# Kernel optimization log

Hardware: AMD Instinct MI355X
Metric: run time of the kernel (lower is better)

## Reference

```python
import jax, jax.numpy as jnp
import numpy as np

N_CODES = 1024  # 'N' in the module: number of codebook entries
DIM = 128       # 'K' in the module: embedding dimension


def setup_inputs() -> dict:
    key = jax.random.key(0)
    k1, k2 = jax.random.split(key)
    x = jax.random.normal(k1, (32, 64, 64, DIM), dtype=jnp.float32)
    # tf.random_uniform_initializer default: uniform in [-0.05, 0.05)
    codebook = jax.random.uniform(k2, (DIM, N_CODES), dtype=jnp.float32,
                                  minval=-0.05, maxval=0.05)
    return {"x": x, "codebook": codebook}


def reference(x, codebook):
    # x: [B, H, W, K]; codebook: [K, N] (codes are columns)
    K = codebook.shape[0]
    flat = x.reshape(-1, K)  # [M, K]
    sim = flat @ codebook    # [M, N]
    dist = (jnp.sum(flat * flat, axis=1, keepdims=True)
            + jnp.sum(codebook * codebook, axis=0)
            - 2.0 * sim)
    idx = jnp.argmin(dist, axis=1)                      # [M]
    q = jnp.take(codebook.T, idx, axis=0).reshape(x.shape)  # gather columns
    # straight-through estimator
    return x + jax.lax.stop_gradient(q - x)
```

## Files before the change

kernel.cpp:

```cpp
#include <hip/hip_runtime.h>
#include <math.h>

typedef _Float16 half8 __attribute__((ext_vector_type(8)));
typedef float    f32x4 __attribute__((ext_vector_type(4)));

#define DIM     128
#define NCODES  1024
#define M_ROWS  (32*64*64)
#define MTILE   128
#define NCHUNK  64
#define M_TEST  3.0e-3f
#define WL_CAP  16384
#define GR      64
#define CSTR    132

__device__ __forceinline__ float sqf(float v) {
    return (float)((double)v * (double)v);
}

__global__ void vq_prep(const float* __restrict__ cb,
                        float* __restrict__ cbT,
                        _Float16* __restrict__ ch,
                        float* __restrict__ cc,
                        int* __restrict__ cnt,
                        unsigned long long* __restrict__ bst) {
    const int b = blockIdx.x;
    if (b < 512) {
        int e = b * 256 + threadIdx.x;
        int n = e & 1023, k = e >> 10;
        float v = cb[k * NCODES + n];
        cbT[n * DIM + k] = v;
        ch[n * DIM + k]  = (_Float16)v;
    } else if (b < 516) {
        int n = (b - 512) * 256 + threadIdx.x;
        float acc = 0.f;
        for (int k = 0; k < DIM; ++k)
            acc = acc + sqf(cb[k * NCODES + n]);
        cc[n] = acc;
        if (n == 0) *cnt = 0;
    } else {
        int s = (b - 516) * 256 + threadIdx.x;
        bst[s] = 0xFFFFFFFFFFFFFFFFull;
    }
}

__device__ __forceinline__ void stage_chunk(const _Float16* __restrict__ ch,
                                            _Float16* lds,
                                            int chunk, int w, int quad, int lane15) {
#pragma unroll
    for (int i = 0; i < 4; ++i) {
        int r = (w << 4) + (i << 2) + quad;
        const _Float16* g = ch + (size_t)(chunk * NCHUNK + r) * DIM
                               + ((lane15 ^ (r & 7)) << 3);
        __builtin_amdgcn_global_load_lds(
            (const __attribute__((address_space(1))) void*)g,
            (__attribute__((address_space(3))) void*)(lds + (w << 11) + (i << 9)),
            16, 0, 0);
    }
}

__global__ __launch_bounds__(256, 2) void vq_gemm(const float* __restrict__ x,
                                                  const _Float16* __restrict__ ch,
                                                  const float* __restrict__ cc,
                                                  int* __restrict__ idx,
                                                  int* __restrict__ cnt,
                                                  int* __restrict__ wl) {
    __shared__ _Float16 bs[2][NCHUNK * DIM];
    __shared__ float ccL[NCODES];

    const int t      = threadIdx.x;
    const int w      = t >> 6;
    const int L      = t & 63;
    const int lane15 = L & 15;
    const int quad   = L >> 4;
    const int rowbase = blockIdx.x * MTILE + w * 32;

    stage_chunk(ch, bs[0], 0, w, quad, lane15);

#pragma unroll
    for (int i = 0; i < 4; ++i)
        ccL[t + 256 * i] = cc[t + 256 * i] + 4.0f;

    half8 af[2][4];
#pragma unroll
    for (int m = 0; m < 2; ++m) {
#pragma unroll
        for (int ks = 0; ks < 4; ++ks) {
            const float* src = x + (size_t)(rowbase + m * 16 + lane15) * DIM
                                 + ks * 32 + quad * 8;
            float4 f0 = *(const float4*)src;
            float4 f1 = *(const float4*)(src + 4);
            half8 h;
            h[0] = (_Float16)f0.x; h[1] = (_Float16)f0.y;
            h[2] = (_Float16)f0.z; h[3] = (_Float16)f0.w;
            h[4] = (_Float16)f1.x; h[5] = (_Float16)f1.y;
            h[6] = (_Float16)f1.z; h[7] = (_Float16)f1.w;
            af[m][ks] = h;
        }
    }

    int roff[4];
#pragma unroll
    for (int ks = 0; ks < 4; ++ks)
        roff[ks] = lane15 * DIM + ((((ks << 2) + quad) ^ (lane15 & 7)) << 3);

    unsigned p1[2][4], p2[2][4];
#pragma unroll
    for (int m = 0; m < 2; ++m)
#pragma unroll
        for (int r = 0; r < 4; ++r) { p1[m][r] = 0xFFFFFFFFu; p2[m][r] = 0xFFFFFFFFu; }

    __syncthreads();

    for (int c = 0; c < NCODES / NCHUNK; ++c) {
        if (c + 1 < NCODES / NCHUNK)
            stage_chunk(ch, bs[(c + 1) & 1], c + 1, w, quad, lane15);

        float cc4[4];
#pragma unroll
        for (int j = 0; j < 4; ++j)
            cc4[j] = ccL[c * NCHUNK + j * 16 + lane15];

        const _Float16* bp = bs[c & 1];
        f32x4 acc[2][4];
#pragma unroll
        for (int m = 0; m < 2; ++m)
#pragma unroll
            for (int j = 0; j < 4; ++j) {
                f32x4 z = {0.f, 0.f, 0.f, 0.f};
                acc[m][j] = z;
            }

#pragma unroll
        for (int ks = 0; ks < 4; ++ks) {
            half8 bf[4];
#pragma unroll
            for (int j = 0; j < 4; ++j)
                bf[j] = *(const half8*)(bp + (j << 11) + roff[ks]);
#pragma unroll
            for (int j = 0; j < 4; ++j)
#pragma unroll
                for (int m = 0; m < 2; ++m)
                    acc[m][j] = __builtin_amdgcn_mfma_f32_16x16x32_f16(af[m][ks], bf[j], acc[m][j], 0, 0, 0);
        }

#pragma unroll
        for (int j = 0; j < 4; ++j) {
            int col = c * NCHUNK + j * 16 + lane15;
#pragma unroll
            for (int m = 0; m < 2; ++m)
#pragma unroll
                for (int r = 0; r < 4; ++r) {
                    float s = fmaf(-2.0f, acc[m][j][r], cc4[j]);
                    s = fmaxf(s, 0.25f);
                    unsigned up = (__float_as_uint(s) & 0xFFFFFC00u) | (unsigned)col;
                    unsigned a  = p1[m][r];
                    unsigned lo = a < up ? a : up;
                    unsigned hi = a < up ? up : a;
                    p1[m][r] = lo;
                    p2[m][r] = p2[m][r] < hi ? p2[m][r] : hi;
                }
        }
        __syncthreads();
    }

#pragma unroll
    for (int m = 0; m < 2; ++m)
#pragma unroll
        for (int r = 0; r < 4; ++r) {
            unsigned a1 = p1[m][r], a2 = p2[m][r];
#pragma unroll
            for (int mask = 1; mask <= 8; mask <<= 1) {
                unsigned b1 = (unsigned)__shfl_xor((int)a1, mask, 64);
                unsigned b2 = (unsigned)__shfl_xor((int)a2, mask, 64);
                unsigned n1 = a1 < b1 ? a1 : b1;
                unsigned hi = a1 < b1 ? b1 : a1;
                unsigned mn = a2 < b2 ? a2 : b2;
                unsigned n2 = hi < mn ? hi : mn;
                a1 = n1; a2 = n2;
            }
            if (lane15 == 0) {
                int row = rowbase + m * 16 + quad * 4 + r;
                idx[row] = (int)(a1 & 0x3FFu);
                float s1 = __uint_as_float(a1 & 0xFFFFFC00u);
                float s2 = __uint_as_float(a2 & 0xFFFFFC00u);
                if (s2 - s1 < M_TEST) {
                    int slot = atomicAdd(cnt, 1);
                    if (slot < WL_CAP) wl[slot] = row;
                }
            }
        }
}

__global__ __launch_bounds__(256, 2) void vq_exact(const float* __restrict__ x,
                                                   const float* __restrict__ cbT,
                                                   const float* __restrict__ cc,
                                                   const int* __restrict__ cnt,
                                                   const int* __restrict__ wl,
                                                   unsigned long long* __restrict__ bst) {
    __shared__ float xsS[GR * CSTR];
    __shared__ float cbS[64 * CSTR];
    __shared__ float xxS[GR];

    const int t  = threadIdx.x;
    const int r4 = t >> 4;
    const int q  = t & 15;

    int count = *cnt;
    if (count > WL_CAP) count = WL_CAP;
    const int ngrp   = (count + GR - 1) / GR;
    const int nitems = ngrp * 4;

    for (int it = blockIdx.x; it < nitems; it += gridDim.x) {
        const int grp = it >> 2;
        const int cq  = it & 3;

        __syncthreads();
#pragma unroll
        for (int j = 0; j < 8; ++j) {
            int e  = t + 256 * j;
            int rr = e >> 5, k4 = e & 31;
            int sl = grp * GR + rr;
            sl = sl < count ? sl : count - 1;
            int rw = wl[sl];
            float4 v = ((const float4*)x)[(size_t)rw * 32 + k4];
            *(float4*)&xsS[rr * CSTR + k4 * 4] = v;
        }
        __syncthreads();

        if (t < GR) {
            const float* xs = &xsS[t * CSTR];
            float r0 = sqf(xs[0]), r1 = sqf(xs[1]), r2 = sqf(xs[2]), r3 = sqf(xs[3]);
            float r4_ = sqf(xs[4]), r5 = sqf(xs[5]), r6 = sqf(xs[6]), r7 = sqf(xs[7]);
#pragma unroll
            for (int k = 8; k < DIM; k += 8) {
                r0 = r0 + sqf(xs[k + 0]); r1 = r1 + sqf(xs[k + 1]);
                r2 = r2 + sqf(xs[k + 2]); r3 = r3 + sqf(xs[k + 3]);
                r4_ = r4_ + sqf(xs[k + 4]); r5 = r5 + sqf(xs[k + 5]);
                r6 = r6 + sqf(xs[k + 6]); r7 = r7 + sqf(xs[k + 7]);
            }
            xxS[t] = ((r0 + r1) + (r2 + r3)) + ((r4_ + r5) + (r6 + r7));
        }
        __syncthreads();

        float xxv[4];
#pragma unroll
        for (int i = 0; i < 4; ++i) xxv[i] = xxS[r4 * 4 + i];

        unsigned long long best[4];
#pragma unroll
        for (int i = 0; i < 4; ++i) best[i] = 0xFFFFFFFFFFFFFFFFull;

        for (int ch = 0; ch < 4; ++ch) {
            const int nb = cq * 256 + ch * 64;
            __syncthreads();
#pragma unroll
            for (int j = 0; j < 8; ++j) {
                int e  = t + 256 * j;
                int ci = e >> 5, k4 = e & 31;
                float4 v = ((const float4*)cbT)[(size_t)(nb + ci) * 32 + k4];
                *(float4*)&cbS[ci * CSTR + k4 * 4] = v;
            }
            __syncthreads();

            float a[4][4];
#pragma unroll
            for (int i = 0; i < 4; ++i)
#pragma unroll
                for (int j = 0; j < 4; ++j) a[i][j] = 0.f;

#pragma unroll 4
            for (int k4 = 0; k4 < 32; ++k4) {
                float4 xv[4], cv[4];
#pragma unroll
                for (int i = 0; i < 4; ++i)
                    xv[i] = *(const float4*)&xsS[(r4 * 4 + i) * CSTR + k4 * 4];
#pragma unroll
                for (int j = 0; j < 4; ++j)
                    cv[j] = *(const float4*)&cbS[(q + 16 * j) * CSTR + k4 * 4];
#pragma unroll
                for (int i = 0; i < 4; ++i)
#pragma unroll
                    for (int j = 0; j < 4; ++j) {
                        float acc = a[i][j];
                        acc = fmaf(cv[j].x, xv[i].x, acc);
                        acc = fmaf(cv[j].y, xv[i].y, acc);
                        acc = fmaf(cv[j].z, xv[i].z, acc);
                        acc = fmaf(cv[j].w, xv[i].w, acc);
                        a[i][j] = acc;
                    }
            }

#pragma unroll
            for (int j = 0; j < 4; ++j) {
                int n = nb + q + 16 * j;
                float ccn = cc[n];
#pragma unroll
                for (int i = 0; i < 4; ++i) {
                    float tt = xxv[i] + ccn;
                    float d  = tt - (a[i][j] + a[i][j]);
                    unsigned u  = __float_as_uint(d);
                    unsigned mk = (unsigned)(((int)u) >> 31);
                    unsigned f  = u ^ (mk | 0x80000000u);
                    unsigned long long key = ((unsigned long long)f << 32) | (unsigned)n;
                    best[i] = key < best[i] ? key : best[i];
                }
            }
        }

#pragma unroll
        for (int i = 0; i < 4; ++i) {
            unsigned long long b = best[i];
#pragma unroll
            for (int mask = 1; mask <= 8; mask <<= 1) {
                unsigned long long o =
                    (unsigned long long)__shfl_xor((long long)b, mask, 64);
                b = o < b ? o : b;
            }
            if (q == 0) {
                int sl = grp * GR + r4 * 4 + i;
                if (sl < count) atomicMin(&bst[sl], b);
            }
        }
    }
}

__global__ void vq_fix(const int* __restrict__ cnt,
                       const int* __restrict__ wl,
                       const unsigned long long* __restrict__ bst,
                       int* __restrict__ idx) {
    int count = *cnt;
    if (count > WL_CAP) count = WL_CAP;
    for (int s = blockIdx.x * 256 + threadIdx.x; s < count; s += gridDim.x * 256)
        idx[wl[s]] = (int)(bst[s] & 0xFFFFFFFFull);
}

__global__ void vq_out(const float* __restrict__ cbT,
                       const int* __restrict__ idx,
                       float* __restrict__ out) {
    size_t e = (size_t)blockIdx.x * 256 + threadIdx.x;
    int row = (int)(e >> 5);
    int k4  = (int)(e & 31);
    ((float4*)out)[e] = ((const float4*)cbT)[(size_t)idx[row] * 32 + k4];
}

extern "C" void kernel_launch(void* const* d_in, const int* in_sizes, int n_in,
                              void* d_out, int out_size, void* d_ws, size_t ws_size,
                              hipStream_t stream) {
    const float* x  = (const float*)d_in[0];
    const float* cb = (const float*)d_in[1];
    float* out = (float*)d_out;

    char* p = (char*)d_ws;
    float*    cbT = (float*)p;               p += NCODES * DIM * sizeof(float);
    _Float16* ch  = (_Float16*)p;            p += NCODES * DIM * sizeof(_Float16);
    float*    cc  = (float*)p;               p += NCODES * sizeof(float);
    int*      idx = (int*)p;                 p += M_ROWS * sizeof(int);
    int*      cnt = (int*)p;                 p += 16 * sizeof(int);
    int*      wl  = (int*)p;                 p += WL_CAP * sizeof(int);
    unsigned long long* bst = (unsigned long long*)p;

    vq_prep<<<580, 256, 0, stream>>>(cb, cbT, ch, cc, cnt, bst);
    vq_gemm<<<M_ROWS / MTILE, 256, 0, stream>>>(x, ch, cc, idx, cnt, wl);
    vq_exact<<<512, 256, 0, stream>>>(x, cbT, cc, cnt, wl, bst);
    vq_fix<<<64, 256, 0, stream>>>(cnt, wl, bst, idx);
    vq_out<<<(M_ROWS * (DIM / 4)) / 256, 256, 0, stream>>>(cbT, idx, out);
}
```

Measured before the change: 186.1 us.

## Software-pipeline MFMA chains with epilogue of previous chunk in vq_gemm

Restructures the codebook chunk loop so the MFMA chain for chunk c+1 is issued before the argmin epilogue of chunk c, using two accumulator sets. This lets the scalar compare/min work overlap with matrix-core latency instead of serializing after it. The ccL table is permuted so each lane reads its four per-chunk norms with one float4 LDS load. The vq_exact grid is doubled. Two accumulator sets raise register pressure, which could limit occupancy at two blocks per CU.

Measured after the change: 196.1 us. +5.4%, slower.

```diff
diff --git a/kernel.cpp b/kernel.cpp
--- a/kernel.cpp
+++ b/kernel.cpp
@@ -59,6 +59,55 @@
     }
 }
 
+#define ZACC(A)                                                               \
+    _Pragma("unroll")                                                         \
+    for (int m_ = 0; m_ < 2; ++m_)                                            \
+        _Pragma("unroll")                                                     \
+        for (int j_ = 0; j_ < 4; ++j_) {                                      \
+            f32x4 z_ = {0.f, 0.f, 0.f, 0.f};                                  \
+            A[m_][j_] = z_;                                                   \
+        }
+
+#define CHAIN(BP, A)                                                          \
+    _Pragma("unroll")                                                         \
+    for (int ks_ = 0; ks_ < 4; ++ks_) {                                       \
+        half8 bf_[4];                                                         \
+        _Pragma("unroll")                                                     \
+        for (int j_ = 0; j_ < 4; ++j_)                                        \
+            bf_[j_] = *(const half8*)((BP) + (j_ << 11) + roff[ks_]);         \
+        _Pragma("unroll")                                                     \
+        for (int j_ = 0; j_ < 4; ++j_)                                        \
+            _Pragma("unroll")                                                 \
+            for (int m_ = 0; m_ < 2; ++m_)                                    \
+                A[m_][j_] = __builtin_amdgcn_mfma_f32_16x16x32_f16(           \
+                    af[m_][ks_], bf_[j_], A[m_][j_], 0, 0, 0);                \
+    }
+
+#define EPI(A, CB, CC4)                                                       \
+    _Pragma("unroll")                                                         \
+    for (int j_ = 0; j_ < 4; ++j_) {                                          \
+        int col_ = (CB) * NCHUNK + j_ * 16 + lane15;                          \
+        _Pragma("unroll")                                                     \
+        for (int m_ = 0; m_ < 2; ++m_)                                        \
+            _Pragma("unroll")                                                 \
+            for (int r_ = 0; r_ < 4; ++r_) {                                  \
+                float s_ = fmaf(-2.0f, A[m_][j_][r_], CC4[j_]);               \
+                s_ = fmaxf(s_, 0.25f);                                        \
+                unsigned up_ = (__float_as_uint(s_) & 0xFFFFFC00u) | (unsigned)col_; \
+                unsigned a_  = p1[m_][r_];                                    \
+                unsigned lo_ = a_ < up_ ? a_ : up_;                           \
+                unsigned hi_ = a_ < up_ ? up_ : a_;                           \
+                p1[m_][r_] = lo_;                                             \
+                p2[m_][r_] = p2[m_][r_] < hi_ ? p2[m_][r_] : hi_;             \
+            }                                                                 \
+    }
+
+#define LOADCC(DST, C)                                                        \
+    {                                                                         \
+        float4 ccv_ = *(const float4*)&ccL[(((C) << 4) + lane15) << 2];       \
+        DST[0] = ccv_.x; DST[1] = ccv_.y; DST[2] = ccv_.z; DST[3] = ccv_.w;   \
+    }
+
 __global__ __launch_bounds__(256, 2) void vq_gemm(const float* __restrict__ x,
                                                   const _Float16* __restrict__ ch,
                                                   const float* __restrict__ cc,
@@ -78,8 +127,12 @@
     stage_chunk(ch, bs[0], 0, w, quad, lane15);
 
 #pragma unroll
-    for (int i = 0; i < 4; ++i)
-        ccL[t + 256 * i] = cc[t + 256 * i] + 4.0f;
+    for (int i = 0; i < 4; ++i) {
+        int e = t + 256 * i;
+        int c = e >> 6, rem = e & 63;
+        int l = rem >> 2, j = rem & 3;
+        ccL[e] = cc[c * 64 + j * 16 + l] + 4.0f;
+    }
 
     half8 af[2][4];
 #pragma unroll
@@ -112,57 +165,36 @@
 
     __syncthreads();
 
-    for (int c = 0; c < NCODES / NCHUNK; ++c) {
-        if (c + 1 < NCODES / NCHUNK)
-            stage_chunk(ch, bs[(c + 1) & 1], c + 1, w, quad, lane15);
-
-        float cc4[4];
-#pragma unroll
-        for (int j = 0; j < 4; ++j)
-            cc4[j] = ccL[c * NCHUNK + j * 16 + lane15];
-
-        const _Float16* bp = bs[c & 1];
-        f32x4 acc[2][4];
-#pragma unroll
-        for (int m = 0; m < 2; ++m)
-#pragma unroll
-            for (int j = 0; j < 4; ++j) {
-                f32x4 z = {0.f, 0.f, 0.f, 0.f};
-                acc[m][j] = z;
-            }
-
-#pragma unroll
-        for (int ks = 0; ks < 4; ++ks) {
-            half8 bf[4];
-#pragma unroll
-            for (int j = 0; j < 4; ++j)
-                bf[j] = *(const half8*)(bp + (j << 11) + roff[ks]);
-#pragma unroll
-            for (int j = 0; j < 4; ++j)
-#pragma unroll
-                for (int m = 0; m < 2; ++m)
-                    acc[m][j] = __builtin_amdgcn_mfma_f32_16x16x32_f16(af[m][ks], bf[j], acc[m][j], 0, 0, 0);
-        }
-
-#pragma unroll
-        for (int j = 0; j < 4; ++j) {
-            int col = c * NCHUNK + j * 16 + lane15;
-#pragma unroll
-            for (int m = 0; m < 2; ++m)
-#pragma unroll
-                for (int r = 0; r < 4; ++r) {
-                    float s = fmaf(-2.0f, acc[m][j][r], cc4[j]);
-                    s = fmaxf(s, 0.25f);
-                    unsigned up = (__float_as_uint(s) & 0xFFFFFC00u) | (unsigned)col;
-                    unsigned a  = p1[m][r];
-                    unsigned lo = a < up ? a : up;
-                    unsigned hi = a < up ? up : a;
-                    p1[m][r] = lo;
-                    p2[m][r] = p2[m][r] < hi ? p2[m][r] : hi;
-                }
-        }
+    f32x4 accA[2][4], accB[2][4];
+    float cc4A[4], cc4B[4];
+
+    stage_chunk(ch, bs[1], 1, w, quad, lane15);
+    LOADCC(cc4A, 0);
+    ZACC(accA);
+    CHAIN(bs[0], accA);
+    __syncthreads();
+
+    for (int c = 1; c < 15; c += 2) {
+        stage_chunk(ch, bs[0], c + 1, w, quad, lane15);
+        LOADCC(cc4B, c);
+        ZACC(accB);
+        CHAIN(bs[1], accB);
+        EPI(accA, c - 1, cc4A);
         __syncthreads();
-    }
+
+        stage_chunk(ch, bs[1], c + 2, w, quad, lane15);
+        LOADCC(cc4A, c + 1);
+        ZACC(accA);
+        CHAIN(bs[0], accA);
+        EPI(accB, c, cc4B);
+        __syncthreads();
+    }
+
+    LOADCC(cc4B, 15);
+    ZACC(accB);
+    CHAIN(bs[1], accB);
+    EPI(accA, 14, cc4A);
+    EPI(accB, 15, cc4B);
 
 #pragma unroll
     for (int m = 0; m < 2; ++m)
@@ -362,7 +394,7 @@
 
     vq_prep<<<580, 256, 0, stream>>>(cb, cbT, ch, cc, cnt, bst);
     vq_gemm<<<M_ROWS / MTILE, 256, 0, stream>>>(x, ch, cc, idx, cnt, wl);
-    vq_exact<<<512, 256, 0, stream>>>(x, cbT, cc, cnt, wl, bst);
+    vq_exact<<<1024, 256, 0, stream>>>(x, cbT, cc, cnt, wl, bst);
     vq_fix<<<64, 256, 0, stream>>>(cnt, wl, bst, idx);
     vq_out<<<(M_ROWS * (DIM / 4)) / 256, 256, 0, stream>>>(cbT, idx, out);
 }
```

## Triple-buffer codebook chunks with one barrier per iteration and vectorized cc loads

Applied to the files above, without the earlier changes.

The GEMM kernel moves from double to triple buffering of codebook chunks in LDS. It prefetches two chunks ahead and uses an explicit vmcnt wait plus a single barrier per iteration instead of two syncthreads. The ccL table is permuted so each lane reads its four code norms with one float4 load. The grid of the exact-refinement kernel is doubled. Extra LDS (48KB for chunk buffers) may limit occupancy at two blocks per CU, and the hand-written waitcnt depends on the exact count of loads issued by stage_chunk.

Measured after the change: 187.9 us. Within noise of the previous version (+1.0%).

```diff
diff --git a/kernel.cpp b/kernel.cpp
--- a/kernel.cpp
+++ b/kernel.cpp
@@ -65,7 +65,7 @@
                                                   int* __restrict__ idx,
                                                   int* __restrict__ cnt,
                                                   int* __restrict__ wl) {
-    __shared__ _Float16 bs[2][NCHUNK * DIM];
+    __shared__ _Float16 bs[3][NCHUNK * DIM];
     __shared__ float ccL[NCODES];
 
     const int t      = threadIdx.x;
@@ -76,10 +76,15 @@
     const int rowbase = blockIdx.x * MTILE + w * 32;
 
     stage_chunk(ch, bs[0], 0, w, quad, lane15);
-
-#pragma unroll
-    for (int i = 0; i < 4; ++i)
-        ccL[t + 256 * i] = cc[t + 256 * i] + 4.0f;
+    stage_chunk(ch, bs[1], 1, w, quad, lane15);
+
+#pragma unroll
+    for (int i = 0; i < 4; ++i) {
+        int e = t + 256 * i;
+        int c = e >> 6, rem = e & 63;
+        int l = rem >> 2, j = rem & 3;
+        ccL[e] = cc[c * 64 + j * 16 + l] + 4.0f;
+    }
 
     half8 af[2][4];
 #pragma unroll
@@ -110,18 +115,25 @@
 #pragma unroll
         for (int r = 0; r < 4; ++r) { p1[m][r] = 0xFFFFFFFFu; p2[m][r] = 0xFFFFFFFFu; }
 
-    __syncthreads();
-
-    for (int c = 0; c < NCODES / NCHUNK; ++c) {
-        if (c + 1 < NCODES / NCHUNK)
-            stage_chunk(ch, bs[(c + 1) & 1], c + 1, w, quad, lane15);
-
-        float cc4[4];
-#pragma unroll
-        for (int j = 0; j < 4; ++j)
-            cc4[j] = ccL[c * NCHUNK + j * 16 + lane15];
-
-        const _Float16* bp = bs[c & 1];
+    const _Float16* bp0 = bs[0];
+    const _Float16* bp1 = bs[1];
+    _Float16*       bp2 = bs[2];
+
+#pragma unroll 1
+    for (int c = 0; c < 16; ++c) {
+        if (c < 15)
+            asm volatile("s_waitcnt vmcnt(4) lgkmcnt(0)" ::: "memory");
+        else
+            asm volatile("s_waitcnt vmcnt(0) lgkmcnt(0)" ::: "memory");
+        __builtin_amdgcn_s_barrier();
+        __builtin_amdgcn_sched_barrier(0);
+
+        if (c < 14)
+            stage_chunk(ch, bp2, c + 2, w, quad, lane15);
+
+        float4 ccv = *(const float4*)&ccL[((c << 4) + lane15) << 2];
+        float cc4[4] = {ccv.x, ccv.y, ccv.z, ccv.w};
+
         f32x4 acc[2][4];
 #pragma unroll
         for (int m = 0; m < 2; ++m)
@@ -136,7 +148,7 @@
             half8 bf[4];
 #pragma unroll
             for (int j = 0; j < 4; ++j)
-                bf[j] = *(const half8*)(bp + (j << 11) + roff[ks]);
+                bf[j] = *(const half8*)(bp0 + (j << 11) + roff[ks]);
 #pragma unroll
             for (int j = 0; j < 4; ++j)
 #pragma unroll
@@ -161,7 +173,9 @@
                     p2[m][r] = p2[m][r] < hi ? p2[m][r] : hi;
                 }
         }
-        __syncthreads();
+
+        _Float16* tmp = (_Float16*)bp0;
+        bp0 = bp1; bp1 = bp2; bp2 = tmp;
     }
 
 #pragma unroll
@@ -362,7 +376,7 @@
 
     vq_prep<<<580, 256, 0, stream>>>(cb, cbT, ch, cc, cnt, bst);
     vq_gemm<<<M_ROWS / MTILE, 256, 0, stream>>>(x, ch, cc, idx, cnt, wl);
-    vq_exact<<<512, 256, 0, stream>>>(x, cbT, cc, cnt, wl, bst);
+    vq_exact<<<1024, 256, 0, stream>>>(x, cbT, cc, cnt, wl, bst);
     vq_fix<<<64, 256, 0, stream>>>(cnt, wl, bst, idx);
     vq_out<<<(M_ROWS * (DIM / 4)) / 256, 256, 0, stream>>>(cbT, idx, out);
 }
```
